# Kernel tuning notes

Measured on AMD Instinct MI355X. Metric: run time of the kernel, lower is better.

The kernel has to match this reference:

```python
import jax, jax.numpy as jnp
import numpy as np
from jax import lax

STRIDE = (1, 1, 1, 1)
PADDING = (1, 1, 1, 1)
DILATION = (1, 1, 1, 1)


def setup_inputs() -> dict:
    key = jax.random.key(0)
    k1, k2, k3 = jax.random.split(key, 3)
    x = jax.random.normal(k1, (4, 32, 8, 24, 24, 24), dtype=jnp.float32)
    # weight layout matches torch ConvTranspose: (C_in, C_out, l_k, d_k, h_k, w_k)
    weight = jax.random.normal(k2, (32, 32, 3, 3, 3, 3), dtype=jnp.float32) * 0.05
    bias = jax.random.normal(k3, (32,), dtype=jnp.float32) * 0.05
    return {"x": x, "weight": weight, "bias": bias}


def _conv_transpose_4d(x, weight):
    # Transposed conv == conv with lhs dilated by stride, kernel spatially
    # flipped, and padding d*(k-1) - p on each side of each spatial dim.
    # Output size per dim: (i-1)*s - 2p + d*(k-1) + 1, identical to the
    # torch module's looped ConvTranspose3d + temporal scatter-add.
    ksp = weight.shape[2:]
    pads = [(d * (k - 1) - p, d * (k - 1) - p)
            for k, p, d in zip(ksp, PADDING, DILATION)]
    w = jnp.flip(weight, axis=(2, 3, 4, 5))  # (C_in, C_out, l, d, h, w)
    return lax.conv_general_dilated(
        x, w,
        window_strides=(1, 1, 1, 1),
        padding=pads,
        lhs_dilation=STRIDE,
        rhs_dilation=DILATION,
        dimension_numbers=("NCLDHW", "IOLDHW", "NCLDHW"),
    )


def reference(x, weight, bias):
    out = _conv_transpose_4d(x, weight)
    return out + bias.reshape(1, -1, 1, 1, 1, 1)
```

## Files before the change

kernel.cpp:

```cpp
#include <hip/hip_runtime.h>

#define NN 4
#define CC 32
#define LL 8
#define DD 24
#define HH 24
#define WW 24

typedef short  bf16x8  __attribute__((ext_vector_type(8)));
typedef float  f32x16  __attribute__((ext_vector_type(16)));
typedef unsigned short ushort8 __attribute__((ext_vector_type(8)));

#define XP_CHUNKS (4 * 4 * 8 * 26 * 26 * 26)
#define XP_ELEMS  (XP_CHUNKS * 8)
#define AS_ELEMS  (4 * 3 * 14 * 64 * 8)

__device__ __forceinline__ unsigned short f2bf(float f) {
    union { float f; unsigned u; } v; v.f = f;
    unsigned r = v.u + 0x7FFFu + ((v.u >> 16) & 1u);
    return (unsigned short)(r >> 16);
}

__device__ __forceinline__ void gload16(const void* g, void* l) {
    __builtin_amdgcn_global_load_lds(
        (const __attribute__((address_space(1))) unsigned int*)g,
        (__attribute__((address_space(3))) unsigned int*)l, 16, 0, 0);
}

__global__ __launch_bounds__(256) void prep_x(const float* __restrict__ x,
                                              unsigned short* __restrict__ xp) {
    const int c  = blockIdx.x * 256 + threadIdx.x;
    const int wp = c % 26;
    const int t1 = c / 26;
    const int hp = t1 % 26;
    const int t2 = t1 / 26;
    const int dp = t2 % 26;
    const int t3 = t2 / 26;
    const int l  = t3 & 7;
    const int t4 = t3 >> 3;
    const int n  = t4 & 3;
    const int cig = t4 >> 2;
    const int dx = dp - 1, hx = hp - 1, wx = wp - 1;
    ushort8 v = {0, 0, 0, 0, 0, 0, 0, 0};
    if ((unsigned)dx < DD && (unsigned)hx < HH && (unsigned)wx < WW) {
        const float* src = x + (((((size_t)n * CC + cig * 8) * LL + l) * DD + dx) * HH + hx) * WW + wx;
#pragma unroll
        for (int ci = 0; ci < 8; ++ci)
            v[ci] = f2bf(src[(size_t)ci * (LL * DD * HH * WW)]);
    }
    *reinterpret_cast<ushort8*>(xp + (size_t)c * 8) = v;
}

__global__ __launch_bounds__(256) void prep_w(const float* __restrict__ wgt,
                                              unsigned short* __restrict__ Ag) {
    const int i  = blockIdx.x * 256 + threadIdx.x;
    const int j  = i & 7;
    const int ln = (i >> 3) & 63;
    const int r  = i >> 9;
    const int s  = r % 14;
    const int r2 = r / 14;
    const int ql = r2 % 3;
    const int cig = r2 / 3;
    const int co = ln & 31, gg = ln >> 5, tau = 2 * s + gg;
    unsigned short v = 0;
    if (tau <= 26)
        v = f2bf(wgt[(size_t)((cig * 8 + j) * CC + co) * 81 + 80 - (ql * 27 + tau)]);
    Ag[i] = v;
}

constexpr int offb(int tau) {
    return ((tau / 9) * 676 + ((tau / 3) % 3) * 26 + (tau % 3)) * 16;
}

__global__ __launch_bounds__(384, 4) void convt4d_main(
    const unsigned short* __restrict__ xp, const unsigned short* __restrict__ Ag,
    const float* __restrict__ bias, float* __restrict__ out)
{
    __shared__ __align__(16) unsigned short xs[2028 * 8];
    __shared__ __align__(16) unsigned short As[896 * 8];

    int bid = (int)blockIdx.x;
    bid = (bid & 7) * 96 + (bid >> 3);
    const int n = bid / (LL * DD);
    const int l = (bid / DD) % LL;
    const int d = bid % DD;

    const int t    = (int)threadIdx.x;
    const int lane = t & 63;
    const int wave = t >> 6;
    const int g    = lane >> 5;
    const int dh   = (lane >> 3) & 3;
    const int dw   = lane & 7;
    const int h0   = wave * 4;

    f32x16 acc[3];
#pragma unroll
    for (int i = 0; i < 3; ++i)
#pragma unroll
        for (int j = 0; j < 16; ++j) acc[i][j] = 0.f;

    const int base0 = ((h0 + dh) * 26 + dw) * 16;
    const char* xsb = (const char*)xs;

#pragma unroll 1
    for (int cig = 0; cig < 4; ++cig) {
#pragma unroll 1
        for (int ql = 0; ql < 3; ++ql) {
            const int lx = l + ql - 1;
            if (lx < 0 || lx >= LL) continue;

            __syncthreads();

            const unsigned short* xsrc =
                xp + (size_t)((((cig * 4 + n) * 8 + lx) * 26 + d)) * 676 * 8;
#pragma unroll
            for (int k0 = 0; k0 < 2028; k0 += 384) {
                int k = k0 + t;
                if (k0 + 384 <= 2028 || k < 2028)
                    gload16(xsrc + (size_t)k * 8, (char*)xs + (size_t)k * 16);
            }
            const unsigned short* asrc = Ag + (size_t)(cig * 3 + ql) * 7168;
#pragma unroll
            for (int k0 = 0; k0 < 896; k0 += 384) {
                int k = k0 + t;
                if (k0 + 384 <= 896 || k < 896)
                    gload16(asrc + (size_t)k * 8, (char*)As + (size_t)k * 16);
            }
            __syncthreads();

#pragma unroll
            for (int s = 0; s < 14; ++s) {
                bf16x8 a = *reinterpret_cast<const bf16x8*>(&As[(s * 64 + lane) * 8]);
                const int t0 = (2 * s     > 26) ? 26 : 2 * s;
                const int t1 = (2 * s + 1 > 26) ? 26 : 2 * s + 1;
                const int off = g ? offb(t1) : offb(t0);
                const char* bp = xsb + (base0 + off);
#pragma unroll
                for (int nt = 0; nt < 3; ++nt) {
                    bf16x8 b = *reinterpret_cast<const bf16x8*>(bp + nt * 128);
                    acc[nt] = __builtin_amdgcn_mfma_f32_32x32x16_bf16(a, b, acc[nt], 0, 0, 0);
                }
            }
        }
    }

#pragma unroll
    for (int r = 0; r < 16; ++r) {
        const int co = (r & 3) + 8 * (r >> 2) + 4 * g;
        const float bv = bias[co];
        size_t ob = (((((size_t)n * CC + co) * LL + l) * DD + d) * HH + (h0 + dh)) * WW + dw;
        out[ob]      = acc[0][r] + bv;
        out[ob + 8]  = acc[1][r] + bv;
        out[ob + 16] = acc[2][r] + bv;
    }
}

extern "C" void kernel_launch(void* const* d_in, const int* in_sizes, int n_in,
                              void* d_out, int out_size, void* d_ws, size_t ws_size,
                              hipStream_t stream) {
    const float* x    = (const float*)d_in[0];
    const float* wgt  = (const float*)d_in[1];
    const float* bias = (const float*)d_in[2];
    float* out = (float*)d_out;

    unsigned short* xp = (unsigned short*)d_ws;
    unsigned short* Ag = xp + XP_ELEMS;

    prep_x<<<XP_CHUNKS / 256, 256, 0, stream>>>(x, xp);
    prep_w<<<AS_ELEMS / 256, 256, 0, stream>>>(wgt, Ag);
    convt4d_main<<<NN * LL * DD, 384, 0, stream>>>(xp, Ag, bias, out);
}
```

Measured before the change: 104.8 us.

## Double-buffer per-depth-plane LDS stages to overlap loads with MFMA

Splits each (cig, ql) stage into three per-d-plane stages with 9-tap weight tiles and double-buffered LDS. The loads for the next stage are issued before computing the current one, so only one barrier is needed per stage. The goal is to hide global-to-LDS load latency behind matrix work and to shrink LDS use per block. The cost is a small rise in padded MFMA work (10 taps per 9 instead of 28 per 27) and more stages with more barriers.

```diff
diff --git a/kernel.cpp b/kernel.cpp
--- a/kernel.cpp
+++ b/kernel.cpp
@@ -13,7 +13,7 @@
 
 #define XP_CHUNKS (4 * 4 * 8 * 26 * 26 * 26)
 #define XP_ELEMS  (XP_CHUNKS * 8)
-#define AS_ELEMS  (4 * 3 * 14 * 64 * 8)
+#define AG_ELEMS  (4 * 3 * 3 * 5 * 64 * 8)
 
 __device__ __forceinline__ unsigned short f2bf(float f) {
     union { float f; unsigned u; } v; v.f = f;
@@ -56,28 +56,27 @@
     const int i  = blockIdx.x * 256 + threadIdx.x;
     const int j  = i & 7;
     const int ln = (i >> 3) & 63;
-    const int r  = i >> 9;
-    const int s  = r % 14;
-    const int r2 = r / 14;
-    const int ql = r2 % 3;
-    const int cig = r2 / 3;
-    const int co = ln & 31, gg = ln >> 5, tau = 2 * s + gg;
+    const int s  = (i >> 9) % 5;
+    const int r  = (i >> 9) / 5;
+    const int qd = r % 3;
+    const int ql = (r / 3) % 3;
+    const int cig = r / 9;
+    const int co = ln & 31, gg = ln >> 5;
+    const int tl = 2 * s + gg;
     unsigned short v = 0;
-    if (tau <= 26)
-        v = f2bf(wgt[(size_t)((cig * 8 + j) * CC + co) * 81 + 80 - (ql * 27 + tau)]);
+    if (tl <= 8) {
+        const int tap = ql * 27 + qd * 9 + tl;
+        v = f2bf(wgt[(size_t)((cig * 8 + j) * CC + co) * 81 + 80 - tap]);
+    }
     Ag[i] = v;
-}
-
-constexpr int offb(int tau) {
-    return ((tau / 9) * 676 + ((tau / 3) % 3) * 26 + (tau % 3)) * 16;
 }
 
 __global__ __launch_bounds__(384, 4) void convt4d_main(
     const unsigned short* __restrict__ xp, const unsigned short* __restrict__ Ag,
     const float* __restrict__ bias, float* __restrict__ out)
 {
-    __shared__ __align__(16) unsigned short xs[2028 * 8];
-    __shared__ __align__(16) unsigned short As[896 * 8];
+    __shared__ __align__(16) unsigned short xs[2][676 * 8];
+    __shared__ __align__(16) unsigned short As[2][320 * 8];
 
     int bid = (int)blockIdx.x;
     bid = (bid & 7) * 96 + (bid >> 3);
@@ -93,6 +92,10 @@
     const int dw   = lane & 7;
     const int h0   = wave * 4;
 
+    const int ql0 = (l == 0) ? 1 : 0;
+    const int nql = 3 - (l == 0) - (l == 7);
+    const int nst = 4 * nql * 3;
+
     f32x16 acc[3];
 #pragma unroll
     for (int i = 0; i < 3; ++i)
@@ -100,46 +103,44 @@
         for (int j = 0; j < 16; ++j) acc[i][j] = 0.f;
 
     const int base0 = ((h0 + dh) * 26 + dw) * 16;
-    const char* xsb = (const char*)xs;
+
+    auto issue = [&](int id, int buf) {
+        const int qd  = id % 3;
+        const int r   = id / 3;
+        const int ql  = ql0 + r % nql;
+        const int cig = r / nql;
+        const int lx  = l + ql - 1;
+        const unsigned short* xsrc =
+            xp + (size_t)((((cig * 4 + n) * 8 + lx) * 26) + (d + qd)) * (676 * 8);
+        gload16(xsrc + (size_t)t * 8, (char*)xs[buf] + (size_t)t * 16);
+        if (t + 384 < 676)
+            gload16(xsrc + (size_t)(t + 384) * 8, (char*)xs[buf] + (size_t)(t + 384) * 16);
+        const unsigned short* asrc = Ag + (size_t)((cig * 3 + ql) * 3 + qd) * 2560;
+        if (t < 320)
+            gload16(asrc + (size_t)t * 8, (char*)As[buf] + (size_t)t * 16);
+    };
+
+    issue(0, 0);
 
 #pragma unroll 1
-    for (int cig = 0; cig < 4; ++cig) {
-#pragma unroll 1
-        for (int ql = 0; ql < 3; ++ql) {
-            const int lx = l + ql - 1;
-            if (lx < 0 || lx >= LL) continue;
+    for (int st = 0; st < nst; ++st) {
+        const int buf = st & 1;
+        __syncthreads();
+        if (st + 1 < nst) issue(st + 1, buf ^ 1);
 
-            __syncthreads();
-
-            const unsigned short* xsrc =
-                xp + (size_t)((((cig * 4 + n) * 8 + lx) * 26 + d)) * 676 * 8;
+        const char* xsb = (const char*)xs[buf];
 #pragma unroll
-            for (int k0 = 0; k0 < 2028; k0 += 384) {
-                int k = k0 + t;
-                if (k0 + 384 <= 2028 || k < 2028)
-                    gload16(xsrc + (size_t)k * 8, (char*)xs + (size_t)k * 16);
-            }
-            const unsigned short* asrc = Ag + (size_t)(cig * 3 + ql) * 7168;
+        for (int s = 0; s < 5; ++s) {
+            bf16x8 a = *reinterpret_cast<const bf16x8*>(&As[buf][(s * 64 + lane) * 8]);
+            const int t0 = 2 * s;
+            const int t1 = (2 * s + 1 > 8) ? 8 : 2 * s + 1;
+            const int tl = g ? t1 : t0;
+            const int off = ((tl / 3) * 26 + (tl % 3)) * 16;
+            const char* bp = xsb + (base0 + off);
 #pragma unroll
-            for (int k0 = 0; k0 < 896; k0 += 384) {
-                int k = k0 + t;
-                if (k0 + 384 <= 896 || k < 896)
-                    gload16(asrc + (size_t)k * 8, (char*)As + (size_t)k * 16);
-            }
-            __syncthreads();
-
-#pragma unroll
-            for (int s = 0; s < 14; ++s) {
-                bf16x8 a = *reinterpret_cast<const bf16x8*>(&As[(s * 64 + lane) * 8]);
-                const int t0 = (2 * s     > 26) ? 26 : 2 * s;
-                const int t1 = (2 * s + 1 > 26) ? 26 : 2 * s + 1;
-                const int off = g ? offb(t1) : offb(t0);
-                const char* bp = xsb + (base0 + off);
-#pragma unroll
-                for (int nt = 0; nt < 3; ++nt) {
-                    bf16x8 b = *reinterpret_cast<const bf16x8*>(bp + nt * 128);
-                    acc[nt] = __builtin_amdgcn_mfma_f32_32x32x16_bf16(a, b, acc[nt], 0, 0, 0);
-                }
+            for (int nt = 0; nt < 3; ++nt) {
+                bf16x8 b = *reinterpret_cast<const bf16x8*>(bp + nt * 128);
+                acc[nt] = __builtin_amdgcn_mfma_f32_32x32x16_bf16(a, b, acc[nt], 0, 0, 0);
             }
         }
     }
@@ -167,6 +168,6 @@
     unsigned short* Ag = xp + XP_ELEMS;
 
     prep_x<<<XP_CHUNKS / 256, 256, 0, stream>>>(x, xp);
-    prep_w<<<AS_ELEMS / 256, 256, 0, stream>>>(wgt, Ag);
+    prep_w<<<AG_ELEMS / 256, 256, 0, stream>>>(wgt, Ag);
     convt4d_main<<<NN * LL * DD, 384, 0, stream>>>(xp, Ag, bias, out);
 }
```

New measurement: 99.14 us. -5.4%, faster.
